# Optimization experiments

Measured on AMD Instinct MI355X. Metric: run time of the kernel, lower is better.

Reference implementation:

```python
import jax, jax.numpy as jnp
import numpy as np

def setup_inputs() -> dict:
    key = jax.random.key(0)
    k1, k2, k3, k4, k5 = jax.random.split(key, 5)
    H = 1024
    B, T = 32, 1024
    hidden = jax.random.normal(k1, (1, B, H), dtype=jnp.float32)
    encoder_outputs = jax.random.normal(k2, (B, T, H), dtype=jnp.float32)
    # nn.Linear(2H, H): weight [H, 2H], bias [H]
    bound = 1.0 / np.sqrt(2 * H)
    W = jax.random.uniform(k3, (H, 2 * H), minval=-bound, maxval=bound, dtype=jnp.float32)
    b = jax.random.uniform(k4, (H,), minval=-bound, maxval=bound, dtype=jnp.float32)
    v = jax.random.uniform(k5, (H,), dtype=jnp.float32)  # torch.rand
    return {"hidden": hidden, "encoder_outputs": encoder_outputs, "W": W, "b": b, "v": v}

def reference(hidden, encoder_outputs, W, b, v):
    B = hidden.shape[1]
    H = hidden.shape[2]
    h = jnp.transpose(hidden, (1, 0, 2)).reshape(B, -1)  # [B, H]
    # Split Linear(2H->H): cat([h_rep, enc]) @ W.T == h @ Wh.T + enc @ We.T
    Wh, We = W[:, :H], W[:, H:]
    # [B,1,H] + [B,T,H] -> [B,T,H]
    pre = jnp.tanh((h @ Wh.T + b)[:, None, :] + jnp.einsum('bth,gh->btg', encoder_outputs, We))
    energies = jnp.einsum('bth,h->bt', pre, v)  # [B, T]
    return jax.nn.softmax(energies, axis=1)[:, None, :]  # [B, 1, T]
```

## Files before the change

kernel.cpp:

```cpp
#include <hip/hip_runtime.h>
#include <hip/hip_fp16.h>

typedef _Float16 half8   __attribute__((ext_vector_type(8)));
typedef _Float16 half4_t __attribute__((ext_vector_type(4)));
typedef float    f32x4   __attribute__((ext_vector_type(4)));

#define HDIM  1024
#define BATCH 32
#define TLEN  1024
#define M_TOT (BATCH * TLEN)

#define BM 128
#define BN 128
#define BKF 64
#define LDA 40

__global__ void prep_k(const float* __restrict__ W, const float* __restrict__ hidden,
                       const float* __restrict__ bias, const float* __restrict__ enc,
                       _Float16* __restrict__ We16, float* __restrict__ q,
                       _Float16* __restrict__ enc16) {
    const int bid = blockIdx.x;
    const int t = threadIdx.x;
    if (bid < 1024) {
        int idx = bid * 256 + t;
        int g  = idx >> 8;
        int k4 = idx & 255;
        float4 f = *reinterpret_cast<const float4*>(W + (size_t)g * 2048 + 1024 + k4 * 4);
        half4_t h;
        h[0] = (_Float16)f.x; h[1] = (_Float16)f.y; h[2] = (_Float16)f.z; h[3] = (_Float16)f.w;
        *reinterpret_cast<half4_t*>(We16 + (size_t)idx * 4) = h;
    } else if (bid < 2048) {
        int g = bid - 1024;
        int wave = t >> 6, lane = t & 63;
        float acc[BATCH];
#pragma unroll
        for (int b = 0; b < BATCH; b++) acc[b] = 0.f;
        const float* wr = W + (size_t)g * 2048;
        for (int h = t; h < HDIM; h += 256) {
            float w = wr[h];
#pragma unroll
            for (int b = 0; b < BATCH; b++) acc[b] = fmaf(w, hidden[b * HDIM + h], acc[b]);
        }
        __shared__ float sm[4 * BATCH];
#pragma unroll
        for (int b = 0; b < BATCH; b++) {
            float s = acc[b];
#pragma unroll
            for (int off = 32; off >= 1; off >>= 1) s += __shfl_xor(s, off);
            if (lane == 0) sm[wave * BATCH + b] = s;
        }
        __syncthreads();
        if (t < BATCH) {
            float s = sm[t] + sm[BATCH + t] + sm[2 * BATCH + t] + sm[3 * BATCH + t];
            q[t * HDIM + g] = s + bias[g];
        }
    } else {
        size_t i = ((size_t)(bid - 2048) * 256 + t) * 8;
        float4 f0 = *reinterpret_cast<const float4*>(enc + i);
        float4 f1 = *reinterpret_cast<const float4*>(enc + i + 4);
        half8 h;
        h[0] = (_Float16)f0.x; h[1] = (_Float16)f0.y; h[2] = (_Float16)f0.z; h[3] = (_Float16)f0.w;
        h[4] = (_Float16)f1.x; h[5] = (_Float16)f1.y; h[6] = (_Float16)f1.z; h[7] = (_Float16)f1.w;
        *reinterpret_cast<half8*>(enc16 + i) = h;
    }
}

__device__ __forceinline__ void async16(const void* g, void* l) {
    __builtin_amdgcn_global_load_lds(
        (const __attribute__((address_space(1))) void*)g,
        (__attribute__((address_space(3))) void*)l, 16, 0, 0);
}

__global__ __launch_bounds__(256)
void attn_gemm_lds_k(const _Float16* __restrict__ enc16,
                     const _Float16* __restrict__ We16,
                     const float* __restrict__ q, const float* __restrict__ v,
                     float* __restrict__ energ) {
    __shared__ _Float16 As[BM * BKF];
    __shared__ _Float16 Bs[BN * BKF];

    const int tid  = threadIdx.x;
    const int id   = blockIdx.x;
    const int xcd  = id & 7;
    const int w    = id >> 3;
    const int m0   = (xcd * 32 + (w >> 3)) * BM;
    const int n0   = (w & 7) * BN;
    const int nblk = w & 7;
    const int wave = tid >> 6;
    const int lane = tid & 63;
    const int quad = lane >> 4;
    const int l16  = lane & 15;
    const int wm   = (wave & 1) * 64;
    const int wn   = (wave >> 1) * 64;

    f32x4 acc[4][4];
#pragma unroll
    for (int i = 0; i < 4; i++)
#pragma unroll
        for (int j = 0; j < 4; j++) acc[i][j] = {0.f, 0.f, 0.f, 0.f};

    const int srow = wave * 32 + (lane >> 3);
    const int scol = ((lane & 7) ^ (lane >> 3)) * 8;
    const _Float16* gA = enc16 + (size_t)(m0 + srow) * HDIM + scol;
    const _Float16* gB = We16  + (size_t)(n0 + srow) * HDIM + scol;
    _Float16* lA = As + wave * 2048;
    _Float16* lB = Bs + wave * 2048;
    const size_t istep = (size_t)8 * HDIM;

#pragma unroll
    for (int ii = 0; ii < 4; ii++) {
        async16(gA + ii * istep, lA + ii * 512);
        async16(gB + ii * istep, lB + ii * 512);
    }
    __syncthreads();

    int aoff[2][4], boff[2][4];
#pragma unroll
    for (int s = 0; s < 2; s++)
#pragma unroll
        for (int i = 0; i < 4; i++) {
            int ra = wm + i * 16 + l16;
            int rb = wn + i * 16 + l16;
            aoff[s][i] = ra * BKF + (((s * 4 + quad) ^ (l16 & 7)) * 8);
            boff[s][i] = rb * BKF + (((s * 4 + quad) ^ (l16 & 7)) * 8);
        }

    for (int k0 = 0; k0 < HDIM; k0 += BKF) {
        half8 af[2][4], bf[2][4];
#pragma unroll
        for (int s = 0; s < 2; s++)
#pragma unroll
            for (int i = 0; i < 4; i++) {
                af[s][i] = *reinterpret_cast<const half8*>(&As[aoff[s][i]]);
                bf[s][i] = *reinterpret_cast<const half8*>(&Bs[boff[s][i]]);
            }
        __syncthreads();

        if (k0 + BKF < HDIM) {
            const int kn = k0 + BKF;
#pragma unroll
            for (int ii = 0; ii < 4; ii++) {
                async16(gA + kn + ii * istep, lA + ii * 512);
                async16(gB + kn + ii * istep, lB + ii * 512);
            }
        }

#pragma unroll
        for (int s = 0; s < 2; s++)
#pragma unroll
            for (int mi = 0; mi < 4; mi++)
#pragma unroll
                for (int ni = 0; ni < 4; ni++)
                    acc[mi][ni] = __builtin_amdgcn_mfma_f32_16x16x32_f16(af[s][mi], bf[s][ni], acc[mi][ni], 0, 0, 0);

        __syncthreads();
    }

    const int bidx = m0 >> 10;
    const int half = wn >> 6;
    float qv[4], vv[4];
#pragma unroll
    for (int ni = 0; ni < 4; ni++) {
        int g = n0 + wn + ni * 16 + l16;
        qv[ni] = q[bidx * HDIM + g];
        vv[ni] = v[g];
    }
#pragma unroll
    for (int mi = 0; mi < 4; mi++) {
#pragma unroll
        for (int r = 0; r < 4; r++) {
            int row = wm + mi * 16 + quad * 4 + r;
            float s = 0.f;
#pragma unroll
            for (int ni = 0; ni < 4; ni++) {
                float pre = acc[mi][ni][r] + qv[ni];
                float e = __expf(2.f * pre);
                float th = 1.f - 2.f / (e + 1.f);
                s = fmaf(th, vv[ni], s);
            }
            s += __shfl_xor(s, 1);
            s += __shfl_xor(s, 2);
            s += __shfl_xor(s, 4);
            s += __shfl_xor(s, 8);
            if (l16 == 0) energ[(size_t)(m0 + row) * 16 + nblk * 2 + half] = s;
        }
    }
}

__global__ __launch_bounds__(256, 2)
void attn_gemm_k(const float* __restrict__ enc, const _Float16* __restrict__ We16,
                 const float* __restrict__ q, const float* __restrict__ v,
                 float* __restrict__ energ) {
    __shared__ _Float16 As[BM * LDA];
    __shared__ _Float16 Bs[BN * LDA];

    const int tid  = threadIdx.x;
    const int m0   = blockIdx.x * BM;
    const int n0   = blockIdx.y * BN;
    const int wave = tid >> 6;
    const int lane = tid & 63;
    const int quad = lane >> 4;
    const int l16  = lane & 15;
    const int wm   = (wave & 1) * 64;
    const int wn   = (wave >> 1) * 64;

    const int srow = tid >> 1;
    const int scol = (tid & 1) * 16;

    f32x4 acc[4][4];
#pragma unroll
    for (int i = 0; i < 4; i++)
#pragma unroll
        for (int j = 0; j < 4; j++) acc[i][j] = {0.f, 0.f, 0.f, 0.f};

    const float*    ag = enc  + (size_t)(m0 + srow) * HDIM + scol;
    const _Float16* bg = We16 + (size_t)(n0 + srow) * HDIM + scol;
    _Float16* aw = &As[srow * LDA + scol];
    _Float16* bw = &Bs[srow * LDA + scol];

    for (int k0 = 0; k0 < HDIM; k0 += 32) {
        float4 a0 = *reinterpret_cast<const float4*>(ag + k0 + 0);
        float4 a1 = *reinterpret_cast<const float4*>(ag + k0 + 4);
        float4 a2 = *reinterpret_cast<const float4*>(ag + k0 + 8);
        float4 a3 = *reinterpret_cast<const float4*>(ag + k0 + 12);
        float4 b0 = *reinterpret_cast<const float4*>(bg + k0);
        float4 b1 = *reinterpret_cast<const float4*>(bg + k0 + 8);

        __syncthreads();

        half8 ha0, ha1;
        ha0[0] = (_Float16)a0.x; ha0[1] = (_Float16)a0.y; ha0[2] = (_Float16)a0.z; ha0[3] = (_Float16)a0.w;
        ha0[4] = (_Float16)a1.x; ha0[5] = (_Float16)a1.y; ha0[6] = (_Float16)a1.z; ha0[7] = (_Float16)a1.w;
        ha1[0] = (_Float16)a2.x; ha1[1] = (_Float16)a2.y; ha1[2] = (_Float16)a2.z; ha1[3] = (_Float16)a2.w;
        ha1[4] = (_Float16)a3.x; ha1[5] = (_Float16)a3.y; ha1[6] = (_Float16)a3.z; ha1[7] = (_Float16)a3.w;
        *reinterpret_cast<half8*>(aw)     = ha0;
        *reinterpret_cast<half8*>(aw + 8) = ha1;
        *reinterpret_cast<float4*>(bw)     = b0;
        *reinterpret_cast<float4*>(bw + 8) = b1;

        __syncthreads();

        half8 af[4], bf[4];
#pragma unroll
        for (int i = 0; i < 4; i++) {
            af[i] = *reinterpret_cast<const half8*>(&As[(wm + i * 16 + l16) * LDA + quad * 8]);
            bf[i] = *reinterpret_cast<const half8*>(&Bs[(wn + i * 16 + l16) * LDA + quad * 8]);
        }
#pragma unroll
        for (int mi = 0; mi < 4; mi++)
#pragma unroll
            for (int ni = 0; ni < 4; ni++)
                acc[mi][ni] = __builtin_amdgcn_mfma_f32_16x16x32_f16(af[mi], bf[ni], acc[mi][ni], 0, 0, 0);
    }

    const int bidx = m0 >> 10;
    const int half = wn >> 6;
    float qv[4], vv[4];
#pragma unroll
    for (int ni = 0; ni < 4; ni++) {
        int g = n0 + wn + ni * 16 + l16;
        qv[ni] = q[bidx * HDIM + g];
        vv[ni] = v[g];
    }
#pragma unroll
    for (int mi = 0; mi < 4; mi++) {
#pragma unroll
        for (int r = 0; r < 4; r++) {
            int row = wm + mi * 16 + quad * 4 + r;
            float s = 0.f;
#pragma unroll
            for (int ni = 0; ni < 4; ni++) {
                float pre = acc[mi][ni][r] + qv[ni];
                float e = __expf(2.f * pre);
                float th = 1.f - 2.f / (e + 1.f);
                s = fmaf(th, vv[ni], s);
            }
            s += __shfl_xor(s, 1);
            s += __shfl_xor(s, 2);
            s += __shfl_xor(s, 4);
            s += __shfl_xor(s, 8);
            if (l16 == 0) energ[(size_t)(m0 + row) * 16 + blockIdx.y * 2 + half] = s;
        }
    }
}

__global__ void softmax_k(const float* __restrict__ energ, float* __restrict__ out) {
    int b = blockIdx.x;
    int t = threadIdx.x;
    int wave = t >> 6, lane = t & 63;
    __shared__ float smax[4], ssum[4];
    float e[4];
#pragma unroll
    for (int i = 0; i < 4; i++) {
        size_t m = (size_t)b * TLEN + t + i * 256;
        const float* p = energ + m * 16;
        f32x4 p0 = *reinterpret_cast<const f32x4*>(p);
        f32x4 p1 = *reinterpret_cast<const f32x4*>(p + 4);
        f32x4 p2 = *reinterpret_cast<const f32x4*>(p + 8);
        f32x4 p3 = *reinterpret_cast<const f32x4*>(p + 12);
        e[i] = ((p0[0] + p0[1]) + (p0[2] + p0[3])) + ((p1[0] + p1[1]) + (p1[2] + p1[3]))
             + ((p2[0] + p2[1]) + (p2[2] + p2[3])) + ((p3[0] + p3[1]) + (p3[2] + p3[3]));
    }
    float m = fmaxf(fmaxf(e[0], e[1]), fmaxf(e[2], e[3]));
#pragma unroll
    for (int off = 32; off >= 1; off >>= 1) m = fmaxf(m, __shfl_xor(m, off));
    if (lane == 0) smax[wave] = m;
    __syncthreads();
    float M = fmaxf(fmaxf(smax[0], smax[1]), fmaxf(smax[2], smax[3]));
    float x[4]; float s = 0.f;
#pragma unroll
    for (int i = 0; i < 4; i++) { x[i] = __expf(e[i] - M); s += x[i]; }
#pragma unroll
    for (int off = 32; off >= 1; off >>= 1) s += __shfl_xor(s, off);
    if (lane == 0) ssum[wave] = s;
    __syncthreads();
    float S = ssum[0] + ssum[1] + ssum[2] + ssum[3];
    float inv = 1.f / S;
#pragma unroll
    for (int i = 0; i < 4; i++) out[b * TLEN + t + i * 256] = x[i] * inv;
}

extern "C" void kernel_launch(void* const* d_in, const int* in_sizes, int n_in,
                              void* d_out, int out_size, void* d_ws, size_t ws_size,
                              hipStream_t stream) {
    const float* hidden = (const float*)d_in[0];
    const float* enc    = (const float*)d_in[1];
    const float* W      = (const float*)d_in[2];
    const float* bias   = (const float*)d_in[3];
    const float* v      = (const float*)d_in[4];
    float* out = (float*)d_out;

    char* ws = (char*)d_ws;
    float*    q     = (float*)ws;
    float*    energ = (float*)(ws + 131072);
    _Float16* We16  = (_Float16*)(ws + 131072 + 2097152);
    _Float16* enc16 = (_Float16*)(ws + 131072 + 2097152 + 2097152);
    const size_t need_fast = 131072 + 2097152 + 2097152 + (size_t)M_TOT * HDIM * 2;

    if (ws_size >= need_fast) {
        prep_k<<<dim3(18432), 256, 0, stream>>>(W, hidden, bias, enc, We16, q, enc16);
        attn_gemm_lds_k<<<dim3(2048), 256, 0, stream>>>(enc16, We16, q, v, energ);
    } else {
        prep_k<<<dim3(2048), 256, 0, stream>>>(W, hidden, bias, enc, We16, q, enc16);
        attn_gemm_k<<<dim3(256, 8), 256, 0, stream>>>(enc, We16, q, v, energ);
    }
    softmax_k<<<dim3(BATCH), 256, 0, stream>>>(energ, out);
}
```

Before: 297.4 us.

## Load weight tile straight from global memory and double-buffer encoder tile in LDS

The GEMM kernel no longer stages the weight (B) tile in shared memory. Each wave reads its B fragments directly from global memory into registers. The encoder (A) tile is kept in LDS, now double-buffered, so the next tile's async copy goes into the other buffer while the current one is read. The goal is to cut LDS traffic and footprint, but each B fragment is now fetched from global/L2 right before its MFMA use with little latency hiding, and waves sharing the same N half fetch it twice.

```diff
diff --git a/kernel.cpp b/kernel.cpp
--- a/kernel.cpp
+++ b/kernel.cpp
@@ -72,12 +72,11 @@
 }
 
 __global__ __launch_bounds__(256)
-void attn_gemm_lds_k(const _Float16* __restrict__ enc16,
-                     const _Float16* __restrict__ We16,
-                     const float* __restrict__ q, const float* __restrict__ v,
-                     float* __restrict__ energ) {
-    __shared__ _Float16 As[BM * BKF];
-    __shared__ _Float16 Bs[BN * BKF];
+void attn_gemm_bg_k(const _Float16* __restrict__ enc16,
+                    const _Float16* __restrict__ We16,
+                    const float* __restrict__ q, const float* __restrict__ v,
+                    float* __restrict__ energ) {
+    __shared__ _Float16 As[2 * BM * BKF];
 
     const int tid  = threadIdx.x;
     const int id   = blockIdx.x;
@@ -102,48 +101,51 @@
     const int srow = wave * 32 + (lane >> 3);
     const int scol = ((lane & 7) ^ (lane >> 3)) * 8;
     const _Float16* gA = enc16 + (size_t)(m0 + srow) * HDIM + scol;
-    const _Float16* gB = We16  + (size_t)(n0 + srow) * HDIM + scol;
-    _Float16* lA = As + wave * 2048;
-    _Float16* lB = Bs + wave * 2048;
+    const int lA = wave * 2048 + (lane & 63) * 8 - (lane & 7) * 8 + (lane & 7) * 8;
     const size_t istep = (size_t)8 * HDIM;
 
-#pragma unroll
-    for (int ii = 0; ii < 4; ii++) {
-        async16(gA + ii * istep, lA + ii * 512);
-        async16(gB + ii * istep, lB + ii * 512);
-    }
-    __syncthreads();
-
-    int aoff[2][4], boff[2][4];
+    int aoff[2][4];
 #pragma unroll
     for (int s = 0; s < 2; s++)
 #pragma unroll
         for (int i = 0; i < 4; i++) {
             int ra = wm + i * 16 + l16;
-            int rb = wn + i * 16 + l16;
             aoff[s][i] = ra * BKF + (((s * 4 + quad) ^ (l16 & 7)) * 8);
-            boff[s][i] = rb * BKF + (((s * 4 + quad) ^ (l16 & 7)) * 8);
-        }
-
-    for (int k0 = 0; k0 < HDIM; k0 += BKF) {
-        half8 af[2][4], bf[2][4];
+        }
+
+    const _Float16* gBf = We16 + (size_t)(n0 + wn + l16) * HDIM + quad * 8;
+
+#pragma unroll
+    for (int ii = 0; ii < 4; ii++)
+        async16(gA + ii * istep, &As[wave * 2048 + ii * 512 + lane * 8]);
+    __syncthreads();
+
+    for (int t = 0; t < 16; t++) {
+        const int k0 = t * BKF;
+        const int pb = (t & 1) * (BM * BKF);
+
+        half8 bf[2][4];
 #pragma unroll
         for (int s = 0; s < 2; s++)
 #pragma unroll
-            for (int i = 0; i < 4; i++) {
-                af[s][i] = *reinterpret_cast<const half8*>(&As[aoff[s][i]]);
-                bf[s][i] = *reinterpret_cast<const half8*>(&Bs[boff[s][i]]);
-            }
-        __syncthreads();
-
-        if (k0 + BKF < HDIM) {
+            for (int i = 0; i < 4; i++)
+                bf[s][i] = *reinterpret_cast<const half8*>(
+                    gBf + (size_t)(i * 16) * HDIM + s * 32 + k0);
+
+        if (t < 15) {
+            const int qb = ((t + 1) & 1) * (BM * BKF);
             const int kn = k0 + BKF;
 #pragma unroll
-            for (int ii = 0; ii < 4; ii++) {
-                async16(gA + kn + ii * istep, lA + ii * 512);
-                async16(gB + kn + ii * istep, lB + ii * 512);
-            }
-        }
+            for (int ii = 0; ii < 4; ii++)
+                async16(gA + kn + ii * istep, &As[qb + wave * 2048 + ii * 512 + lane * 8]);
+        }
+
+        half8 af[2][4];
+#pragma unroll
+        for (int s = 0; s < 2; s++)
+#pragma unroll
+            for (int i = 0; i < 4; i++)
+                af[s][i] = *reinterpret_cast<const half8*>(&As[pb + aoff[s][i]]);
 
 #pragma unroll
         for (int s = 0; s < 2; s++)
@@ -339,7 +341,7 @@
 
     if (ws_size >= need_fast) {
         prep_k<<<dim3(18432), 256, 0, stream>>>(W, hidden, bias, enc, We16, q, enc16);
-        attn_gemm_lds_k<<<dim3(2048), 256, 0, stream>>>(enc16, We16, q, v, energ);
+        attn_gemm_bg_k<<<dim3(2048), 256, 0, stream>>>(enc16, We16, q, v, energ);
     } else {
         prep_k<<<dim3(2048), 256, 0, stream>>>(W, hidden, bias, enc, We16, q, enc16);
         attn_gemm_k<<<dim3(256, 8), 256, 0, stream>>>(enc, We16, q, v, energ);
```

Result: slower. 368.8 us (+24.0%).
